# Performance work log

Hardware: AMD Instinct MI355X
Metric: run time of the kernel (lower is better)

The kernel has to match this reference:

```python
import jax, jax.numpy as jnp
import numpy as np

V, C, DFF, NH, NL, KS, OUT = 256, 192, 768, 2, 6, 3, 192
B, T, W = 64, 512, 4
DH = C // NH
PAD = KS // 2
DN = ('NCH', 'OIH', 'NCH')


def _rel_to_abs(x):
    # [b,h,l,2l-1] -> [b,h,l,l]  (VITS _relative_position_to_absolute_position)
    b, h, l, _ = x.shape
    x = jnp.pad(x, ((0, 0), (0, 0), (0, 0), (0, 1)))
    x = x.reshape(b, h, l * 2 * l)
    x = jnp.pad(x, ((0, 0), (0, 0), (0, l - 1)))
    x = x.reshape(b, h, l + 1, 2 * l - 1)
    return x[:, :, :l, l - 1:]


def _abs_to_rel(x):
    # [b,h,l,l] -> [b,h,l,2l-1]  (VITS _absolute_position_to_relative_position)
    b, h, l, _ = x.shape
    x = jnp.pad(x, ((0, 0), (0, 0), (0, 0), (0, l - 1)))
    x = x.reshape(b, h, l * (2 * l - 1))
    x = jnp.pad(x, ((0, 0), (0, 0), (l, 0)))
    x = x.reshape(b, h, l, 2 * l)
    return x[:, :, :, 1:]


def _get_rel_emb(emb, length):
    # emb: [2W+1, DH] -> [2*length-1, DH]
    pad_len = max(length - (W + 1), 0)
    start = max(W + 1 - length, 0)
    padded = jnp.pad(emb, ((pad_len, pad_len), (0, 0)))
    return padded[start:start + 2 * length - 1]


def _ln(x, g, b):
    mu = jnp.mean(x, -1, keepdims=True)
    var = jnp.mean(jnp.square(x - mu), -1, keepdims=True)
    return (x - mu) * jax.lax.rsqrt(var + 1e-5) * g + b


def setup_inputs():
    key = jax.random.key(0)
    ks = jax.random.split(key, 12)
    n = lambda k, s, std: jax.random.normal(k, s, jnp.float32) * std
    return dict(
        tokens=jax.random.randint(ks[0], (B, T), 0, V),
        x_lengths=jnp.full((B,), T, dtype=jnp.int32),
        emb_w=n(ks[1], (V, C), C ** -0.5),
        wqkv=n(ks[2], (NL, 3, C, C), 0.02),
        bqkv=jnp.zeros((NL, 3, C), jnp.float32),
        wo=n(ks[3], (NL, C, C), 0.02),
        bo=jnp.zeros((NL, C), jnp.float32),
        rel_k=n(ks[4], (NL, 2 * W + 1, DH), DH ** -0.5),
        rel_v=n(ks[5], (NL, 2 * W + 1, DH), DH ** -0.5),
        ln1_g=jnp.ones((NL, C), jnp.float32),
        ln1_b=jnp.zeros((NL, C), jnp.float32),
        ln2_g=jnp.ones((NL, C), jnp.float32),
        ln2_b=jnp.zeros((NL, C), jnp.float32),
        ffn_w1=n(ks[6], (NL, DFF, C, KS), 0.02),
        ffn_b1=jnp.zeros((NL, DFF), jnp.float32),
        ffn_w2=n(ks[7], (NL, C, DFF, KS), 0.02),
        ffn_b2=jnp.zeros((NL, C), jnp.float32),
        proj_w=n(ks[8], (2 * OUT, C), 0.02),
        proj_b=jnp.zeros((2 * OUT,), jnp.float32),
    )


def reference(tokens, x_lengths, emb_w, wqkv, bqkv, wo, bo, rel_k, rel_v,
              ln1_g, ln1_b, ln2_g, ln2_b, ffn_w1, ffn_b1, ffn_w2, ffn_b2,
              proj_w, proj_b):
    x = emb_w[tokens] * (C ** 0.5)                       # [B,T,C]
    mask = (jnp.arange(T)[None, :] < x_lengths[:, None]).astype(x.dtype)  # [B,T]
    bias = jnp.where((mask[:, None, :, None] * mask[:, None, None, :]) > 0.0, 0.0, -1e4)
    x = x * mask[..., None]
    inv_sqrt_d = DH ** -0.5
    for l in range(NL):
        q = jnp.einsum('btc,oc->bto', x, wqkv[l, 0]) + bqkv[l, 0]
        k = jnp.einsum('btc,oc->bto', x, wqkv[l, 1]) + bqkv[l, 1]
        v = jnp.einsum('btc,oc->bto', x, wqkv[l, 2]) + bqkv[l, 2]
        q = q.reshape(B, T, NH, DH).transpose(0, 2, 1, 3)  # [B,H,T,D]
        k = k.reshape(B, T, NH, DH).transpose(0, 2, 1, 3)
        v = v.reshape(B, T, NH, DH).transpose(0, 2, 1, 3)
        scores = jnp.einsum('bhtd,bhsd->bhts', q, k) * inv_sqrt_d
        rk = _get_rel_emb(rel_k[l], T)                     # [2T-1, D]
        rel_logits = jnp.einsum('bhtd,md->bhtm', q * inv_sqrt_d, rk)
        scores = scores + _rel_to_abs(rel_logits)
        p = jax.nn.softmax(scores + bias, axis=-1)
        o = jnp.einsum('bhts,bhsd->bhtd', p, v)
        o = o + jnp.einsum('bhtm,md->bhtd', _abs_to_rel(p), _get_rel_emb(rel_v[l], T))
        o = o.transpose(0, 2, 1, 3).reshape(B, T, C)
        y = jnp.einsum('btc,oc->bto', o, wo[l]) + bo[l]
        x = _ln(x + y, ln1_g[l], ln1_b[l])
        h = jax.lax.conv_general_dilated((x * mask[..., None]).transpose(0, 2, 1),
                                         ffn_w1[l], (1,), [(PAD, PAD)],
                                         dimension_numbers=DN) + ffn_b1[l][None, :, None]
        h = jax.nn.relu(h) * mask[:, None, :]
        h = jax.lax.conv_general_dilated(h, ffn_w2[l], (1,), [(PAD, PAD)],
                                         dimension_numbers=DN) + ffn_b2[l][None, :, None]
        y = h.transpose(0, 2, 1) * mask[..., None]
        x = _ln(x + y, ln2_g[l], ln2_b[l])
    x = x * mask[..., None]
    stats = (jnp.einsum('btc,oc->bto', x, proj_w) + proj_b) * mask[..., None]
    m, logs = jnp.split(stats, 2, axis=-1)
    x_mask = mask[:, None, :]
    return x.transpose(0, 2, 1), m.transpose(0, 2, 1), logs.transpose(0, 2, 1), x_mask
```

## Files before the change

kernel.cpp:

```cpp
#include <hip/hip_runtime.h>
#include <hip/hip_bf16.h>

typedef __hip_bfloat16 bf16;
typedef __attribute__((ext_vector_type(8))) short short8;
typedef __attribute__((ext_vector_type(4))) float f32x4;

#define NB 64
#define NT 512
#define NC 192
#define NHEAD 2
#define NDH 96
#define NLAYER 6
#define NDFF 768
#define NW 4

constexpr int MROWS = NB * NT;
constexpr size_t MC = (size_t)MROWS * NC;
constexpr size_t MCB = MC * 4;
constexpr float QSC = 0.10206207261596575f * 1.4426950408889634f;

__device__ __forceinline__ float us2f(unsigned short x) { return __uint_as_float((unsigned)x << 16); }
__device__ __forceinline__ unsigned short f2b(float f) {
    bf16 h = __float2bfloat16(f);
    return *reinterpret_cast<unsigned short*>(&h);
}

__global__ __launch_bounds__(256) void cvt_frag_plain(const float* __restrict__ s, bf16* __restrict__ d,
                                                      int L, int N, int K) {
    int i = blockIdx.x * 256 + threadIdx.x;
    int total = L * (N / 16) * (K / 32) * 64;
    if (i >= total) return;
    int lane = i & 63;
    int tile = i >> 6;
    int nbk = K / 32;
    int kb = tile % nbk;
    int rest = tile / nbk;
    int nb = rest % (N / 16);
    int l = rest / (N / 16);
    int li = lane & 15, g = lane >> 4;
    const float* src = s + ((size_t)l * N + nb * 16 + li) * K + kb * 32 + g * 8;
    bf16* dst = d + (size_t)i * 8;
#pragma unroll
    for (int u = 0; u < 8; u++) dst[u] = __float2bfloat16(src[u]);
}
__global__ __launch_bounds__(256) void cvt_frag_conv(const float* __restrict__ s, bf16* __restrict__ d,
                                                     int L, int N, int C) {
    int i = blockIdx.x * 256 + threadIdx.x;
    int total = L * 3 * (N / 16) * (C / 32) * 64;
    if (i >= total) return;
    int lane = i & 63;
    int tile = i >> 6;
    int nbk = C / 32;
    int kb = tile % nbk;
    int rest = tile / nbk;
    int nb = rest % (N / 16);
    int rest2 = rest / (N / 16);
    int dk = rest2 % 3;
    int l = rest2 / 3;
    int li = lane & 15, g = lane >> 4;
    const float* src = s + (((size_t)l * N + nb * 16 + li) * C + kb * 32 + g * 8) * 3 + dk;
    bf16* dst = d + (size_t)i * 8;
#pragma unroll
    for (int u = 0; u < 8; u++) dst[u] = __float2bfloat16(src[u * 3]);
}

__global__ __launch_bounds__(256) void embed_kernel(const int* __restrict__ tok,
                                                    const int* __restrict__ lens,
                                                    const float* __restrict__ emb,
                                                    bf16* __restrict__ xb) {
    int idx = blockIdx.x * 256 + threadIdx.x;
    if (idx >= (int)MC) return;
    int c = idx % NC;
    int m = idx / NC;
    int t = m % NT, b = m / NT;
    float v = emb[tok[m] * NC + c] * 13.856406460551018f;
    if (t >= lens[b]) v = 0.f;
    xb[idx] = __float2bfloat16(v);
}

enum GMode { GM_QKV = 0, GM_CONV1 = 2, GM_PROJ = 4 };

template <int MODE, int NTOT, int KC, int TAPS>
__global__ __launch_bounds__(256) void gemm_mfma(const bf16* __restrict__ A,
                                                 const bf16* __restrict__ W,
                                                 const float* __restrict__ bias,
                                                 const int* __restrict__ lens,
                                                 float* __restrict__ of,
                                                 bf16* __restrict__ ob1,
                                                 bf16* __restrict__ ob2,
                                                 bf16* __restrict__ ob3) {
    constexpr int RA = (TAPS == 3) ? 130 : 128;
    constexpr int NBN = NTOT / 16;
    constexpr int NBK = KC / 32;
    __shared__ unsigned short As[RA * 40];
    const int tid = threadIdx.x;
    const int w = tid >> 6, lane = tid & 63;
    const int g = lane >> 4, li = lane & 15;
    const int n0 = blockIdx.x * 64;
    const int m0 = blockIdx.y * 128;
    const int b = m0 >> 9, t0 = m0 & 511;
    const int len = lens[b];
    const int nbBase = n0 >> 4;
    const unsigned short* Au = (const unsigned short*)A;
    const unsigned short* Wu = (const unsigned short*)W;

    f32x4 acc[2][4];
#pragma unroll
    for (int a = 0; a < 2; a++)
#pragma unroll
        for (int s = 0; s < 4; s++) acc[a][s] = (f32x4){0.f, 0.f, 0.f, 0.f};

#pragma unroll 1
    for (int k0 = 0; k0 < KC; k0 += 32) {
        const int kb = k0 >> 5;
        __syncthreads();
        for (int c = tid; c < RA * 2; c += 256) {
            int i = c >> 1, hf = (c & 1) * 16;
            int t = t0 + i - (TAPS == 3 ? 1 : 0);
            bool valid = (t >= 0) && (t < NT);
            if constexpr (MODE == GM_CONV1) valid = valid && (t < len);
            short8 v0{}, v1{};
            if (valid) {
                const unsigned short* src = Au + ((size_t)(b * NT + t) * KC + k0 + hf);
                v0 = *(const short8*)src;
                v1 = *(const short8*)(src + 8);
            }
            *(short8*)&As[i * 40 + hf] = v0;
            *(short8*)&As[i * 40 + hf + 8] = v1;
        }
        __syncthreads();
#pragma unroll
        for (int dk = 0; dk < TAPS; dk++) {
            short8 af0 = *(const short8*)&As[(w * 32 + li + dk) * 40 + g * 8];
            short8 af1 = *(const short8*)&As[(w * 32 + 16 + li + dk) * 40 + g * 8];
#pragma unroll
            for (int sub = 0; sub < 4; sub++) {
                short8 bfr = *(const short8*)(Wu +
                    ((((size_t)(dk * NBN + nbBase + sub)) * NBK + kb) << 9) + (lane << 3));
                acc[0][sub] = __builtin_amdgcn_mfma_f32_16x16x32_bf16(af0, bfr, acc[0][sub], 0, 0, 0);
                acc[1][sub] = __builtin_amdgcn_mfma_f32_16x16x32_bf16(af1, bfr, acc[1][sub], 0, 0, 0);
            }
        }
    }

#pragma unroll
    for (int sub = 0; sub < 4; sub++) {
        int n = n0 + sub * 16 + li;
        float bv = bias[n];
#pragma unroll
        for (int a = 0; a < 2; a++) {
#pragma unroll
            for (int rr = 0; rr < 4; rr++) {
                int t = t0 + w * 32 + a * 16 + g * 4 + rr;
                size_t m = (size_t)(b * NT + t);
                float vv = acc[a][sub][rr] + bv;
                if constexpr (MODE == GM_QKV) {
                    int iw = n / NC;
                    int cc = n - iw * NC;
                    int hh = cc >= NDH ? 1 : 0;
                    int d = cc - hh * NDH;
                    int bh = b * NHEAD + hh;
                    if (iw == 0) ob1[((size_t)bh * NT + t) * NDH + d] = __float2bfloat16(vv * QSC);
                    else if (iw == 1) ob2[((size_t)bh * NT + t) * NDH + d] = __float2bfloat16(vv);
                    else ob3[((size_t)bh * NDH + d) * NT + t] = __float2bfloat16(vv);
                } else if constexpr (MODE == GM_CONV1) {
                    vv = vv > 0.f ? vv : 0.f;
                    if (t >= len) vv = 0.f;
                    ob1[m * NDFF + n] = __float2bfloat16(vv);
                } else {
                    if (t >= len) vv = 0.f;
                    int half = n >= 192 ? 1 : 0;
                    int cc = n - half * 192;
                    of[(size_t)(half + 1) * MC + ((size_t)b * NC + cc) * NT + t] = vv;
                }
            }
        }
    }
}

template <int KC, int TAPS, bool MASKY, int BM>
__global__ __launch_bounds__(512, 4) void gemm_ln(const bf16* __restrict__ A,
                                                  const bf16* __restrict__ W,
                                                  const float* __restrict__ bias,
                                                  const int* __restrict__ lens,
                                                  const float* __restrict__ lng,
                                                  const float* __restrict__ lnb,
                                                  bf16* __restrict__ xb) {
    constexpr int RA = BM + ((TAPS == 3) ? 2 : 0);
    constexpr int NSTEP = KC / 32;
    constexpr int NBN = 12;
    constexpr int NBK = KC / 32;
    constexpr int AR = BM / 32;
    __shared__ unsigned short As[RA * 40];
    __shared__ float rsm[BM][4];
    __shared__ float rsq[BM][4];
    const int tid = threadIdx.x;
    const int lane = tid & 63;
    const int g = lane >> 4, li = lane & 15;
    const int w = tid >> 6;
    const int wr = w & 1, wc = w >> 1;
    const int m0 = blockIdx.x * BM;
    const int b = m0 >> 9, t0 = m0 & 511;
    const int len = lens[b];
    const unsigned short* Au = (const unsigned short*)A;
    const unsigned short* Wu = (const unsigned short*)W;
    unsigned short* Xu = (unsigned short*)xb;

    const int ai = tid >> 1, ahf = (tid & 1) * 16;
    const int at = t0 + ai - (TAPS == 3 ? 1 : 0);
    const bool aon = (tid < RA * 2);
    const bool avalid = aon && (at >= 0) && (at < NT);

    short8 ra0{}, ra1{};
    short8 bcur[TAPS][3], bnxt[TAPS][3];

    f32x4 acc[AR][3];
#pragma unroll
    for (int ar = 0; ar < AR; ar++)
#pragma unroll
        for (int sub = 0; sub < 3; sub++) acc[ar][sub] = (f32x4){0.f, 0.f, 0.f, 0.f};

    if (avalid) {
        const unsigned short* src = Au + ((size_t)(b * NT + at) * KC + 0 + ahf);
        ra0 = *(const short8*)src;
        ra1 = *(const short8*)(src + 8);
    }
#pragma unroll
    for (int dk = 0; dk < TAPS; dk++)
#pragma unroll
        for (int sub = 0; sub < 3; sub++)
            bcur[dk][sub] = *(const short8*)(Wu +
                ((((size_t)(dk * NBN + wc * 3 + sub)) * NBK) << 9) + (lane << 3));
    if (aon) {
        short8 z{};
        *(short8*)&As[ai * 40 + ahf] = avalid ? ra0 : z;
        *(short8*)&As[ai * 40 + ahf + 8] = avalid ? ra1 : z;
    }

#pragma unroll 1
    for (int s = 0; s < NSTEP; s++) {
        __syncthreads();
        if (s + 1 < NSTEP) {
            int k0 = (s + 1) * 32;
            if (avalid) {
                const unsigned short* src = Au + ((size_t)(b * NT + at) * KC + k0 + ahf);
                ra0 = *(const short8*)src;
                ra1 = *(const short8*)(src + 8);
            }
#pragma unroll
            for (int dk = 0; dk < TAPS; dk++)
#pragma unroll
                for (int sub = 0; sub < 3; sub++)
                    bnxt[dk][sub] = *(const short8*)(Wu +
                        ((((size_t)(dk * NBN + wc * 3 + sub)) * NBK + (s + 1)) << 9) + (lane << 3));
        }
#pragma unroll
        for (int dk = 0; dk < TAPS; dk++) {
            short8 af[AR];
#pragma unroll
            for (int ar = 0; ar < AR; ar++)
                af[ar] = *(const short8*)&As[(wr * (BM / 2) + ar * 16 + li + dk) * 40 + g * 8];
#pragma unroll
            for (int sub = 0; sub < 3; sub++) {
#pragma unroll
                for (int ar = 0; ar < AR; ar++)
                    acc[ar][sub] = __builtin_amdgcn_mfma_f32_16x16x32_bf16(af[ar], bcur[dk][sub], acc[ar][sub], 0, 0, 0);
            }
        }
        __syncthreads();
        if (s + 1 < NSTEP) {
            if (aon) {
                short8 z{};
                *(short8*)&As[ai * 40 + ahf] = avalid ? ra0 : z;
                *(short8*)&As[ai * 40 + ahf + 8] = avalid ? ra1 : z;
            }
#pragma unroll
            for (int dk = 0; dk < TAPS; dk++)
#pragma unroll
                for (int sub = 0; sub < 3; sub++) bcur[dk][sub] = bnxt[dk][sub];
        }
    }

    float biasv[3], gv[3], bbv[3];
#pragma unroll
    for (int sub = 0; sub < 3; sub++) {
        int n = wc * 48 + sub * 16 + li;
        biasv[sub] = bias[n];
        gv[sub] = lng[n];
        bbv[sub] = lnb[n];
    }
    float psm[AR][4], psq[AR][4];
#pragma unroll
    for (int ar = 0; ar < AR; ar++) {
#pragma unroll
        for (int rr = 0; rr < 4; rr++) {
            int r = wr * (BM / 2) + ar * 16 + 4 * g + rr;
            int t = t0 + r;
            size_t m = (size_t)(b * NT + t);
            float sm = 0.f, sq = 0.f;
#pragma unroll
            for (int sub = 0; sub < 3; sub++) {
                int n = wc * 48 + sub * 16 + li;
                float y = acc[ar][sub][rr] + biasv[sub];
                if (MASKY && t >= len) y = 0.f;
                float rres = y + us2f(Xu[m * NC + n]);
                acc[ar][sub][rr] = rres;
                sm += rres;
                sq += rres * rres;
            }
            psm[ar][rr] = sm;
            psq[ar][rr] = sq;
        }
    }
#pragma unroll
    for (int off = 1; off < 16; off <<= 1) {
#pragma unroll
        for (int ar = 0; ar < AR; ar++)
#pragma unroll
            for (int rr = 0; rr < 4; rr++) {
                psm[ar][rr] += __shfl_xor(psm[ar][rr], off);
                psq[ar][rr] += __shfl_xor(psq[ar][rr], off);
            }
    }
    if (li == 0) {
#pragma unroll
        for (int ar = 0; ar < AR; ar++)
#pragma unroll
            for (int rr = 0; rr < 4; rr++) {
                int r = wr * (BM / 2) + ar * 16 + 4 * g + rr;
                rsm[r][wc] = psm[ar][rr];
                rsq[r][wc] = psq[ar][rr];
            }
    }
    __syncthreads();
#pragma unroll
    for (int ar = 0; ar < AR; ar++) {
#pragma unroll
        for (int rr = 0; rr < 4; rr++) {
            int r = wr * (BM / 2) + ar * 16 + 4 * g + rr;
            int t = t0 + r;
            size_t m = (size_t)(b * NT + t);
            float sm = rsm[r][0] + rsm[r][1] + rsm[r][2] + rsm[r][3];
            float sq = rsq[r][0] + rsq[r][1] + rsq[r][2] + rsq[r][3];
            float mu = sm * (1.f / NC);
            float var = fmaxf(sq * (1.f / NC) - mu * mu, 0.f);
            float rs = rsqrtf(var + 1e-5f);
#pragma unroll
            for (int sub = 0; sub < 3; sub++) {
                int n = wc * 48 + sub * 16 + li;
                float o = (acc[ar][sub][rr] - mu) * rs * gv[sub] + bbv[sub];
                Xu[m * NC + n] = f2b(o);
            }
        }
    }
}

__global__ __launch_bounds__(256, 4) void attn_mfma(const bf16* __restrict__ q,
                                                    const bf16* __restrict__ k,
                                                    const bf16* __restrict__ v,
                                                    const float* __restrict__ relk,
                                                    const float* __restrict__ relv,
                                                    const int* __restrict__ lens,
                                                    bf16* __restrict__ o) {
    __shared__ __align__(16) char pool[40448];
    unsigned short* Kt = (unsigned short*)pool;
    unsigned short* Vt = (unsigned short*)(pool + 13312);
    unsigned short* Pt = (unsigned short*)(pool + 27136);
    unsigned short* Pb = (unsigned short*)(pool + 36352);
    unsigned short* Qt = (unsigned short*)pool;
    unsigned short* Rk = (unsigned short*)(pool + 13312);

    const int bh = blockIdx.x, qt = blockIdx.y;
    const int b = bh >> 1, h = bh & 1;
    const int q0 = qt * 64;
    const int tid = threadIdx.x;
    const int w = tid >> 6, lane = tid & 63;
    const int g = lane >> 4, li = lane & 15;
    const int len = lens[b];
    const bool anymask = (len < NT);

    const unsigned short* qg = (const unsigned short*)q + (size_t)bh * NT * NDH;
    const unsigned short* kg = (const unsigned short*)k + (size_t)bh * NT * NDH;
    const unsigned short* vg = (const unsigned short*)v + (size_t)bh * NDH * NT;

    for (int c = tid; c < 64 * 12; c += 256) {
        int r = c / 12, seg = (c % 12) * 8;
        *(short8*)&Qt[r * 104 + seg] = *(const short8*)(qg + (size_t)(q0 + r) * NDH + seg);
    }
    for (int c = tid; c < 16 * 96; c += 256) {
        int dd = c / 96, d = c - (c / 96) * 96;
        Rk[dd * 104 + d] = (dd < 9) ? f2b(relk[dd * 96 + d]) : (unsigned short)0;
    }
    for (int c = tid; c < 4 * 16 * 32; c += 256) Pb[c] = 0;
    __syncthreads();

    f32x4 racc = (f32x4){0.f, 0.f, 0.f, 0.f};
    short8 qf[3];
#pragma unroll
    for (int kk = 0; kk < 3; kk++) {
        qf[kk] = *(const short8*)&Qt[(w * 16 + li) * 104 + kk * 32 + g * 8];
        short8 bfr = *(const short8*)&Rk[li * 104 + kk * 32 + g * 8];
        racc = __builtin_amdgcn_mfma_f32_16x16x32_bf16(qf[kk], bfr, racc, 0, 0, 0);
    }
    short8 rvf[6];
#pragma unroll
    for (int ds = 0; ds < 6; ds++) {
#pragma unroll
        for (int i = 0; i < 8; i++) {
            int j = g * 8 + i;
            int d = ds * 16 + li;
            unsigned short u = (j < 9) ? f2b(relv[j * 96 + d]) : (unsigned short)0;
            rvf[ds][i] = (short)u;
        }
    }
    short8 bones;
#pragma unroll
    for (int i = 0; i < 8; i++) bones[i] = (li == 0) ? (short)0x3F80 : (short)0;
    __syncthreads();

    float m_run[4];
    f32x4 Oa[7];
#pragma unroll
    for (int rr = 0; rr < 4; rr++) m_run[rr] = -1e30f;
#pragma unroll
    for (int ds = 0; ds < 7; ds++) Oa[ds] = (f32x4){0.f, 0.f, 0.f, 0.f};

    const int wrow0 = q0 + w * 16;

    for (int s0 = 0; s0 < NT; s0 += 64) {
        for (int c = tid; c < 64 * 12; c += 256) {
            int ss = c / 12, seg = (c % 12) * 8;
            *(short8*)&Kt[ss * 104 + seg] = *(const short8*)(kg + (size_t)(s0 + ss) * NDH + seg);
        }
        for (int c = tid; c < 96 * 8; c += 256) {
            int d = c >> 3, seg = (c & 7) * 8;
            *(short8*)&Vt[d * 72 + seg] = *(const short8*)(vg + (size_t)d * NT + s0 + seg);
        }
        __syncthreads();

        const bool band = (s0 <= wrow0 + 15 + NW) && (s0 + 63 >= wrow0 - NW);

        f32x4 acc[4];
#pragma unroll
        for (int sub = 0; sub < 4; sub++) acc[sub] = (f32x4){0.f, 0.f, 0.f, 0.f};
        __builtin_amdgcn_s_setprio(1);
#pragma unroll
        for (int kk = 0; kk < 3; kk++) {
#pragma unroll
            for (int sub = 0; sub < 4; sub++) {
                short8 bfr = *(const short8*)&Kt[(sub * 16 + li) * 104 + kk * 32 + g * 8];
                acc[sub] = __builtin_amdgcn_mfma_f32_16x16x32_bf16(qf[kk], bfr, acc[sub], 0, 0, 0);
            }
        }
        __builtin_amdgcn_s_setprio(0);

        if (band) {
#pragma unroll
            for (int sub = 0; sub < 4; sub++) {
#pragma unroll
                for (int rr = 0; rr < 4; rr++) {
                    int scol = s0 + sub * 16 + li;
                    int qrow = wrow0 + 4 * g + rr;
                    int dd = scol - qrow;
                    float rv = __shfl(racc[rr], g * 16 + dd + NW);
                    if (dd >= -NW && dd <= NW) acc[sub][rr] += rv;
                }
            }
        }
        if (anymask) {
#pragma unroll
            for (int sub = 0; sub < 4; sub++) {
#pragma unroll
                for (int rr = 0; rr < 4; rr++) {
                    int scol = s0 + sub * 16 + li;
                    int qrow = wrow0 + 4 * g + rr;
                    if (scol >= len || qrow >= len) acc[sub][rr] -= 14427.0f;
                }
            }
        }
        float pmr[4];
#pragma unroll
        for (int rr = 0; rr < 4; rr++) {
            pmr[rr] = fmaxf(fmaxf(acc[0][rr], acc[1][rr]), fmaxf(acc[2][rr], acc[3][rr]));
        }
        float growth = fmaxf(fmaxf(pmr[0] - m_run[0], pmr[1] - m_run[1]),
                             fmaxf(pmr[2] - m_run[2], pmr[3] - m_run[3]));
        if (__any(growth > 11.54f)) {
#pragma unroll
            for (int off = 1; off < 16; off <<= 1)
#pragma unroll
                for (int rr = 0; rr < 4; rr++) pmr[rr] = fmaxf(pmr[rr], __shfl_xor(pmr[rr], off));
#pragma unroll
            for (int rr = 0; rr < 4; rr++) {
                float mn = fmaxf(m_run[rr], pmr[rr]);
                float scf = exp2f(m_run[rr] - mn);
                m_run[rr] = mn;
#pragma unroll
                for (int ds = 0; ds < 7; ds++) Oa[ds][rr] *= scf;
            }
        }
#pragma unroll
        for (int sub = 0; sub < 4; sub++)
#pragma unroll
            for (int rr = 0; rr < 4; rr++)
                acc[sub][rr] = exp2f(acc[sub][rr] - m_run[rr]);

#pragma unroll
        for (int sub = 0; sub < 4; sub++)
#pragma unroll
            for (int rr = 0; rr < 4; rr++)
                Pt[w * 1152 + (4 * g + rr) * 72 + sub * 16 + li] = f2b(acc[sub][rr]);

        __builtin_amdgcn_s_setprio(1);
#pragma unroll
        for (int kk = 0; kk < 2; kk++) {
            short8 pa = *(const short8*)&Pt[w * 1152 + li * 72 + kk * 32 + g * 8];
#pragma unroll
            for (int ds = 0; ds < 6; ds++) {
                short8 bv = *(const short8*)&Vt[(ds * 16 + li) * 72 + kk * 32 + g * 8];
                Oa[ds] = __builtin_amdgcn_mfma_f32_16x16x32_bf16(pa, bv, Oa[ds], 0, 0, 0);
            }
            Oa[6] = __builtin_amdgcn_mfma_f32_16x16x32_bf16(pa, bones, Oa[6], 0, 0, 0);
        }
        __builtin_amdgcn_s_setprio(0);

        if (band) {
            for (int j = g; j < 9; j += 4) {
                int u = wrow0 + li + j - NW - s0;
                unsigned short pv_ = (u >= 0 && u < 64) ? Pt[w * 1152 + li * 72 + u] : (unsigned short)0;
                Pb[w * 512 + li * 32 + j] = pv_;
            }
            short8 pband = *(const short8*)&Pb[w * 512 + li * 32 + g * 8];
#pragma unroll
            for (int ds = 0; ds < 6; ds++)
                Oa[ds] = __builtin_amdgcn_mfma_f32_16x16x32_bf16(pband, rvf[ds], Oa[ds], 0, 0, 0);
        }
        __syncthreads();
    }

    float invl[4];
#pragma unroll
    for (int rr = 0; rr < 4; rr++) invl[rr] = 1.f / __shfl(Oa[6][rr], lane & 48);
#pragma unroll
    for (int ds = 0; ds < 6; ds++)
#pragma unroll
        for (int rr = 0; rr < 4; rr++) {
            int qrow = wrow0 + 4 * g + rr;
            o[((size_t)(b * NT + qrow)) * NC + h * 96 + ds * 16 + li] =
                __float2bfloat16(Oa[ds][rr] * invl[rr]);
        }
}

__global__ __launch_bounds__(256) void xpose_kernel(const bf16* __restrict__ xb,
                                                    const int* __restrict__ lens,
                                                    float* __restrict__ out) {
    int idx = blockIdx.x * 256 + threadIdx.x;
    if (idx >= (int)MC) return;
    int t = idx % NT;
    int bc = idx / NT;
    int c = bc % NC;
    int b = bc / NC;
    float v = (t < lens[b]) ? us2f(((const unsigned short*)xb)[((size_t)b * NT + t) * NC + c]) : 0.f;
    out[idx] = v;
}

__global__ __launch_bounds__(256) void mask_kernel(const int* __restrict__ lens, float* __restrict__ out) {
    int idx = blockIdx.x * 256 + threadIdx.x;
    if (idx >= NB * NT) return;
    int t = idx % NT;
    int b = idx / NT;
    out[idx] = (t < lens[b]) ? 1.f : 0.f;
}

extern "C" void kernel_launch(void* const* d_in, const int* in_sizes, int n_in,
                              void* d_out, int out_size, void* d_ws, size_t ws_size,
                              hipStream_t stream) {
    (void)in_sizes; (void)n_in; (void)out_size; (void)ws_size;
    const int* tok = (const int*)d_in[0];
    const int* lens = (const int*)d_in[1];
    const float* emb = (const float*)d_in[2];
    const float* wqkv = (const float*)d_in[3];
    const float* bqkv = (const float*)d_in[4];
    const float* wo = (const float*)d_in[5];
    const float* bo = (const float*)d_in[6];
    const float* relk = (const float*)d_in[7];
    const float* relv = (const float*)d_in[8];
    const float* ln1g = (const float*)d_in[9];
    const float* ln1b = (const float*)d_in[10];
    const float* ln2g = (const float*)d_in[11];
    const float* ln2b = (const float*)d_in[12];
    const float* fw1 = (const float*)d_in[13];
    const float* fb1 = (const float*)d_in[14];
    const float* fw2 = (const float*)d_in[15];
    const float* fb2 = (const float*)d_in[16];
    const float* pw = (const float*)d_in[17];
    const float* pb = (const float*)d_in[18];
    float* out = (float*)d_out;

    char* wsb = (char*)d_ws;
    bf16* xb = (bf16*)(wsb + 2 * MCB);
    bf16* qb = (bf16*)(wsb + 2 * MCB + MCB / 2);
    bf16* kb = qb + MC;
    bf16* vb = kb + MC;
    bf16* ob = vb + MC;
    bf16* hB = qb;
    bf16* pwqkv = ob + MC;
    bf16* pwo = pwqkv + (size_t)NLAYER * 3 * NC * NC;
    bf16* pw1 = pwo + (size_t)NLAYER * NC * NC;
    bf16* pw2 = pw1 + (size_t)NLAYER * 3 * NDFF * NC;
    bf16* pproj = pw2 + (size_t)NLAYER * 3 * NC * NDFF;

    {
        int n1 = NLAYER * 36 * 6 * 64;
        cvt_frag_plain<<<(n1 + 255) / 256, 256, 0, stream>>>(wqkv, pwqkv, NLAYER, 576, 192);
        int n2 = NLAYER * 12 * 6 * 64;
        cvt_frag_plain<<<(n2 + 255) / 256, 256, 0, stream>>>(wo, pwo, NLAYER, 192, 192);
        int n3 = 1 * 24 * 6 * 64;
        cvt_frag_plain<<<(n3 + 255) / 256, 256, 0, stream>>>(pw, pproj, 1, 384, 192);
        int n4 = NLAYER * 3 * 48 * 6 * 64;
        cvt_frag_conv<<<(n4 + 255) / 256, 256, 0, stream>>>(fw1, pw1, NLAYER, 768, 192);
        int n5 = NLAYER * 3 * 12 * 24 * 64;
        cvt_frag_conv<<<(n5 + 255) / 256, 256, 0, stream>>>(fw2, pw2, NLAYER, 192, 768);
    }

    embed_kernel<<<(int)((MC + 255) / 256), 256, 0, stream>>>(tok, lens, emb, xb);

    for (int l = 0; l < NLAYER; l++) {
        gemm_mfma<GM_QKV, 576, 192, 1><<<dim3(9, 256), 256, 0, stream>>>(
            xb, pwqkv + (size_t)l * 3 * NC * NC, bqkv + (size_t)l * 3 * NC, lens,
            nullptr, qb, kb, vb);
        attn_mfma<<<dim3(NB * NHEAD, 8), 256, 0, stream>>>(
            qb, kb, vb, relk + (size_t)l * (2 * NW + 1) * NDH,
            relv + (size_t)l * (2 * NW + 1) * NDH, lens, ob);
        gemm_ln<192, 1, false, 64><<<512, 512, 0, stream>>>(
            ob, pwo + (size_t)l * NC * NC, bo + (size_t)l * NC, lens,
            ln1g + (size_t)l * NC, ln1b + (size_t)l * NC, xb);
        gemm_mfma<GM_CONV1, 768, 192, 3><<<dim3(12, 256), 256, 0, stream>>>(
            xb, pw1 + (size_t)l * 3 * NDFF * NC, fb1 + (size_t)l * NDFF, lens,
            nullptr, hB, nullptr, nullptr);
        gemm_ln<768, 3, true, 64><<<512, 512, 0, stream>>>(
            hB, pw2 + (size_t)l * 3 * NC * NDFF, fb2 + (size_t)l * NC, lens,
            ln2g + (size_t)l * NC, ln2b + (size_t)l * NC, xb);
    }

    gemm_mfma<GM_PROJ, 384, 192, 1><<<dim3(6, 256), 256, 0, stream>>>(
        xb, pproj, pb, lens, out, nullptr, nullptr, nullptr);
    xpose_kernel<<<(int)((MC + 255) / 256), 256, 0, stream>>>(xb, lens, out);
    mask_kernel<<<(NB * NT + 255) / 256, 256, 0, stream>>>(lens, out + 3 * MC);
}
```

Baseline: 1.369 ms.

## Prefetch K/V tiles into registers in attention; widen conv1 GEMM N tile

The attention kernel now loads the next K and V tiles from global memory into registers while the current tile is being computed, and writes them to shared memory after the closing barrier. This is meant to hide global-load latency behind the MFMA work. Separately, the gemm_mfma template gains a BN parameter, and the conv1 GEMM uses a 128-wide N tile over half as many blocks. That reuses each staged A tile across more output columns, at the cost of more accumulator registers and fewer blocks.

New measurement: 1.639 ms. 1.2x slower.

```diff
diff --git a/kernel.cpp b/kernel.cpp
--- a/kernel.cpp
+++ b/kernel.cpp
@@ -80,7 +80,7 @@
 
 enum GMode { GM_QKV = 0, GM_CONV1 = 2, GM_PROJ = 4 };
 
-template <int MODE, int NTOT, int KC, int TAPS>
+template <int MODE, int NTOT, int KC, int TAPS, int BN>
 __global__ __launch_bounds__(256) void gemm_mfma(const bf16* __restrict__ A,
                                                  const bf16* __restrict__ W,
                                                  const float* __restrict__ bias,
@@ -92,11 +92,12 @@
     constexpr int RA = (TAPS == 3) ? 130 : 128;
     constexpr int NBN = NTOT / 16;
     constexpr int NBK = KC / 32;
+    constexpr int NSUB = BN / 16;
     __shared__ unsigned short As[RA * 40];
     const int tid = threadIdx.x;
     const int w = tid >> 6, lane = tid & 63;
     const int g = lane >> 4, li = lane & 15;
-    const int n0 = blockIdx.x * 64;
+    const int n0 = blockIdx.x * BN;
     const int m0 = blockIdx.y * 128;
     const int b = m0 >> 9, t0 = m0 & 511;
     const int len = lens[b];
@@ -104,11 +105,11 @@
     const unsigned short* Au = (const unsigned short*)A;
     const unsigned short* Wu = (const unsigned short*)W;
 
-    f32x4 acc[2][4];
+    f32x4 acc[2][NSUB];
 #pragma unroll
     for (int a = 0; a < 2; a++)
 #pragma unroll
-        for (int s = 0; s < 4; s++) acc[a][s] = (f32x4){0.f, 0.f, 0.f, 0.f};
+        for (int s = 0; s < NSUB; s++) acc[a][s] = (f32x4){0.f, 0.f, 0.f, 0.f};
 
 #pragma unroll 1
     for (int k0 = 0; k0 < KC; k0 += 32) {
@@ -134,7 +135,7 @@
             short8 af0 = *(const short8*)&As[(w * 32 + li + dk) * 40 + g * 8];
             short8 af1 = *(const short8*)&As[(w * 32 + 16 + li + dk) * 40 + g * 8];
 #pragma unroll
-            for (int sub = 0; sub < 4; sub++) {
+            for (int sub = 0; sub < NSUB; sub++) {
                 short8 bfr = *(const short8*)(Wu +
                     ((((size_t)(dk * NBN + nbBase + sub)) * NBK + kb) << 9) + (lane << 3));
                 acc[0][sub] = __builtin_amdgcn_mfma_f32_16x16x32_bf16(af0, bfr, acc[0][sub], 0, 0, 0);
@@ -144,7 +145,7 @@
     }
 
 #pragma unroll
-    for (int sub = 0; sub < 4; sub++) {
+    for (int sub = 0; sub < NSUB; sub++) {
         int n = n0 + sub * 16 + li;
         float bv = bias[n];
 #pragma unroll
@@ -383,6 +384,27 @@
     const unsigned short* kg = (const unsigned short*)k + (size_t)bh * NT * NDH;
     const unsigned short* vg = (const unsigned short*)v + (size_t)bh * NDH * NT;
 
+    short8 kr[3], vr[3];
+    const int kc0 = tid, kc1 = tid + 256, kc2 = tid + 512;
+    const int vc0 = tid, vc1 = tid + 256, vc2 = tid + 512;
+
+    auto load_tile = [&](int s0) {
+        kr[0] = *(const short8*)(kg + (size_t)(s0 + kc0 / 12) * NDH + (kc0 % 12) * 8);
+        kr[1] = *(const short8*)(kg + (size_t)(s0 + kc1 / 12) * NDH + (kc1 % 12) * 8);
+        kr[2] = *(const short8*)(kg + (size_t)(s0 + kc2 / 12) * NDH + (kc2 % 12) * 8);
+        vr[0] = *(const short8*)(vg + (size_t)(vc0 >> 3) * NT + s0 + (vc0 & 7) * 8);
+        vr[1] = *(const short8*)(vg + (size_t)(vc1 >> 3) * NT + s0 + (vc1 & 7) * 8);
+        vr[2] = *(const short8*)(vg + (size_t)(vc2 >> 3) * NT + s0 + (vc2 & 7) * 8);
+    };
+    auto store_tile = [&]() {
+        *(short8*)&Kt[(kc0 / 12) * 104 + (kc0 % 12) * 8] = kr[0];
+        *(short8*)&Kt[(kc1 / 12) * 104 + (kc1 % 12) * 8] = kr[1];
+        *(short8*)&Kt[(kc2 / 12) * 104 + (kc2 % 12) * 8] = kr[2];
+        *(short8*)&Vt[(vc0 >> 3) * 72 + (vc0 & 7) * 8] = vr[0];
+        *(short8*)&Vt[(vc1 >> 3) * 72 + (vc1 & 7) * 8] = vr[1];
+        *(short8*)&Vt[(vc2 >> 3) * 72 + (vc2 & 7) * 8] = vr[2];
+    };
+
     for (int c = tid; c < 64 * 12; c += 256) {
         int r = c / 12, seg = (c % 12) * 8;
         *(short8*)&Qt[r * 104 + seg] = *(const short8*)(qg + (size_t)(q0 + r) * NDH + seg);
@@ -393,6 +415,8 @@
     }
     for (int c = tid; c < 4 * 16 * 32; c += 256) Pb[c] = 0;
     __syncthreads();
+
+    load_tile(0);
 
     f32x4 racc = (f32x4){0.f, 0.f, 0.f, 0.f};
     short8 qf[3];
@@ -417,6 +441,7 @@
 #pragma unroll
     for (int i = 0; i < 8; i++) bones[i] = (li == 0) ? (short)0x3F80 : (short)0;
     __syncthreads();
+    store_tile();
 
     float m_run[4];
     f32x4 Oa[7];
@@ -428,15 +453,8 @@
     const int wrow0 = q0 + w * 16;
 
     for (int s0 = 0; s0 < NT; s0 += 64) {
-        for (int c = tid; c < 64 * 12; c += 256) {
-            int ss = c / 12, seg = (c % 12) * 8;
-            *(short8*)&Kt[ss * 104 + seg] = *(const short8*)(kg + (size_t)(s0 + ss) * NDH + seg);
-        }
-        for (int c = tid; c < 96 * 8; c += 256) {
-            int d = c >> 3, seg = (c & 7) * 8;
-            *(short8*)&Vt[d * 72 + seg] = *(const short8*)(vg + (size_t)d * NT + s0 + seg);
-        }
         __syncthreads();
+        if (s0 + 64 < NT) load_tile(s0 + 64);
 
         const bool band = (s0 <= wrow0 + 15 + NW) && (s0 + 63 >= wrow0 - NW);
 
@@ -536,6 +554,7 @@
                 Oa[ds] = __builtin_amdgcn_mfma_f32_16x16x32_bf16(pband, rvf[ds], Oa[ds], 0, 0, 0);
         }
         __syncthreads();
+        if (s0 + 64 < NT) store_tile();
     }
 
     float invl[4];
@@ -626,7 +645,7 @@
     embed_kernel<<<(int)((MC + 255) / 256), 256, 0, stream>>>(tok, lens, emb, xb);
 
     for (int l = 0; l < NLAYER; l++) {
-        gemm_mfma<GM_QKV, 576, 192, 1><<<dim3(9, 256), 256, 0, stream>>>(
+        gemm_mfma<GM_QKV, 576, 192, 1, 64><<<dim3(9, 256), 256, 0, stream>>>(
             xb, pwqkv + (size_t)l * 3 * NC * NC, bqkv + (size_t)l * 3 * NC, lens,
             nullptr, qb, kb, vb);
         attn_mfma<<<dim3(NB * NHEAD, 8), 256, 0, stream>>>(
@@ -635,7 +654,7 @@
         gemm_ln<192, 1, false, 64><<<512, 512, 0, stream>>>(
             ob, pwo + (size_t)l * NC * NC, bo + (size_t)l * NC, lens,
             ln1g + (size_t)l * NC, ln1b + (size_t)l * NC, xb);
-        gemm_mfma<GM_CONV1, 768, 192, 3><<<dim3(12, 256), 256, 0, stream>>>(
+        gemm_mfma<GM_CONV1, 768, 192, 3, 128><<<dim3(6, 256), 256, 0, stream>>>(
             xb, pw1 + (size_t)l * 3 * NDFF * NC, fb1 + (size_t)l * NDFF, lens,
             nullptr, hB, nullptr, nullptr);
         gemm_ln<768, 3, true, 64><<<512, 512, 0, stream>>>(
@@ -643,7 +662,7 @@
             ln2g + (size_t)l * NC, ln2b + (size_t)l * NC, xb);
     }
 
-    gemm_mfma<GM_PROJ, 384, 192, 1><<<dim3(6, 256), 256, 0, stream>>>(
+    gemm_mfma<GM_PROJ, 384, 192, 1, 64><<<dim3(6, 256), 256, 0, stream>>>(
         xb, pproj, pb, lens, out, nullptr, nullptr, nullptr);
     xpose_kernel<<<(int)((MC + 255) / 256), 256, 0, stream>>>(xb, lens, out);
     mask_kernel<<<(NB * NT + 255) / 256, 256, 0, stream>>>(lens, out + 3 * MC);
```
